# Performance work log

Hardware: AMD Instinct MI355X
Metric: run time of the kernel (lower is better)

The kernel has to match this reference:

```python
import jax, jax.numpy as jnp
import numpy as np

E, T, IN, OUT, GS = 8, 2048, 2048, 2048, 64


def setup_inputs() -> dict:
    key = jax.random.key(0)
    k1, k2, k3, k4, k5 = jax.random.split(key, 5)
    x = jax.random.normal(k1, (T, IN), dtype=jnp.float32)
    # int4 codes in [0,16): stored unpacked as int32 for the reference
    qweight = jax.random.randint(k2, (E, IN, OUT), 0, 16, dtype=jnp.int32)
    G = IN // GS  # quant groups along the reduction dim
    scales = jax.random.uniform(k3, (E, G, OUT), jnp.float32, minval=0.005, maxval=0.02)
    zeros = jax.random.normal(k4, (E, G, OUT), jnp.float32) * 0.01
    scales_and_zeros = jnp.stack([scales, zeros], axis=-1)  # [E, G, OUT, 2]
    # tokens sorted by expert: per-expert counts are diffs of sorted cut points, sum == T
    cuts = jnp.sort(jax.random.randint(k5, (E - 1,), 0, T + 1, dtype=jnp.int32))
    bounds = jnp.concatenate([jnp.zeros((1,), jnp.int32), cuts, jnp.full((1,), T, jnp.int32)])
    tokens_per_expert = jnp.diff(bounds).astype(jnp.int32)  # [E]
    return {
        "x": x,
        "qweight": qweight,
        "scales_and_zeros": scales_and_zeros,
        "tokens_per_expert": tokens_per_expert,
        "group_size": GS,
    }


def reference(x, qweight, scales_and_zeros, tokens_per_expert, group_size):
    """Grouped (per-expert) int4 dequant + GEMM over an expert-sorted token matrix.

    Math of aten._weight_int4pack_mm per expert e over each quant group g:
        W_e[k, n] = (q_e[k, n] - 8) * scale_e[g, n] + zero_e[g, n],  g = k // group_size
        out[rows_e] = x[rows_e] @ W_e
    where rows_e is the contiguous slice given by cumsum(tokens_per_expert).
    """
    n_exp, in_f, out_f = qweight.shape
    n_tok = x.shape[0]
    G = in_f // group_size

    # dequantize all expert weights: [E, IN, OUT]
    q = qweight.reshape(n_exp, G, group_size, out_f).astype(x.dtype)
    scales = scales_and_zeros[..., 0][:, :, None, :]  # [E, G, 1, OUT]
    zeros = scales_and_zeros[..., 1][:, :, None, :]   # [E, G, 1, OUT]
    W = ((q - 8.0) * scales + zeros).reshape(n_exp, in_f, out_f)

    # expert id per token from the cumsum boundaries (tokens are expert-sorted)
    cum = jnp.cumsum(tokens_per_expert)                                # [E]
    eid = jnp.searchsorted(cum, jnp.arange(n_tok), side="right")       # [T]
    onehot = (eid[:, None] == jnp.arange(n_exp)[None, :]).astype(x.dtype)  # [T, E]

    # dispatch -> per-expert GEMM -> combine (jit-safe grouped GEMM)
    xe = jnp.einsum("te,ti->eti", onehot, x)       # [E, T, IN]
    ye = jnp.einsum("eti,eio->eto", xe, W)         # [E, T, OUT]
    out = jnp.einsum("te,eto->to", onehot, ye)     # [T, OUT]
    return out
```

## Files before the change

### kernel.cpp

```cpp
#include <hip/hip_runtime.h>
#include <hip/hip_bf16.h>

constexpr int NE  = 8;
constexpr int T   = 2048;
constexpr int IN  = 2048;
constexpr int OUT = 2048;
constexpr int GS  = 64;
constexpr int G   = IN / GS;

constexpr int BM = 128;
constexpr int BN = 64;
constexpr int BK = 64;
constexpr int KSPLIT = 2;
constexpr int KCH = IN / KSPLIT;
constexpr int LDA = BK + 8;
constexpr int LDB = BK + 8;

using short8  = __attribute__((ext_vector_type(8))) short;
using floatx4 = __attribute__((ext_vector_type(4))) float;

__global__ __launch_bounds__(256, 4)
void hqq_grouped_gemm(const float* __restrict__ x,
                      const int*   __restrict__ qw,
                      const float* __restrict__ snz,
                      const int*   __restrict__ tpe,
                      float* __restrict__ out) {
    const int tid = threadIdx.x;
    const int e   = blockIdx.z >> 1;
    const int kh  = blockIdx.z & 1;
    const int tm  = blockIdx.y;
    const int n0  = blockIdx.x * BN;

    int b0 = 0;
    for (int i = 0; i < NE; ++i) {
        int c = tpe[i];
        if (i < e) b0 += c;
    }
    const int b1 = b0 + tpe[e];
    const int row0 = b0 + tm * BM;
    if (row0 >= b1) return;

    __shared__ __hip_bfloat16 As[BM][LDA];
    __shared__ __hip_bfloat16 Bs[BN][LDB];

    floatx4 acc[2][4];
#pragma unroll
    for (int i = 0; i < 2; ++i)
#pragma unroll
        for (int j = 0; j < 4; ++j)
            acc[i][j] = (floatx4){0.f, 0.f, 0.f, 0.f};

    const int a_c  = (tid & 15) * 4;
    const int a_r0 = tid >> 4;

    const int bn_ = tid & 63;
    const int bk0 = (tid >> 6) * 8;

    const int lane = tid & 63;
    const int wid  = tid >> 6;
    const int wm = wid * 32;
    const int lm = lane & 15;
    const int lk = (lane >> 4) * 8;

    const int*    qbase  = qw + (size_t)e * IN * OUT + n0 + bn_;
    const float2* szbase = (const float2*)snz + (size_t)e * G * OUT + n0 + bn_;

    const int kbeg = kh * KCH;
    const int kend = kbeg + KCH;

    for (int k0 = kbeg; k0 < kend; k0 += BK) {
#pragma unroll
        for (int it = 0; it < 8; ++it) {
            const int r   = a_r0 + it * 16;
            const int row = row0 + r;
            float4 v = {0.f, 0.f, 0.f, 0.f};
            if (row < b1)
                v = *(const float4*)(x + (size_t)row * IN + k0 + a_c);
            union { unsigned long long u; __hip_bfloat162 h2[2]; } pa;
            pa.h2[0] = __float22bfloat162_rn(float2{v.x, v.y});
            pa.h2[1] = __float22bfloat162_rn(float2{v.z, v.w});
            *(unsigned long long*)&As[r][a_c] = pa.u;
        }

        const int g = k0 >> 6;
        const float2 sz = szbase[(size_t)g * OUT];
        const float s = sz.x;
        const float c = sz.y - 8.0f * s;
#pragma unroll
        for (int p = 0; p < 2; ++p) {
            const int k8 = bk0 + p * 32;
            const int* qp = qbase + (size_t)(k0 + k8) * OUT;
            float f[8];
#pragma unroll
            for (int j = 0; j < 8; ++j) {
                const int q = qp[(size_t)j * OUT];
                f[j] = (float)q * s + c;
            }
            union { short8 v; __hip_bfloat162 h2[4]; } pb;
#pragma unroll
            for (int j = 0; j < 4; ++j)
                pb.h2[j] = __float22bfloat162_rn(float2{f[2 * j], f[2 * j + 1]});
            *(short8*)&Bs[bn_][k8] = pb.v;
        }

        __syncthreads();

#pragma unroll
        for (int ks = 0; ks < BK; ks += 32) {
            short8 af[2], bfr[4];
#pragma unroll
            for (int i = 0; i < 2; ++i)
                af[i] = *(const short8*)&As[wm + i * 16 + lm][ks + lk];
#pragma unroll
            for (int j = 0; j < 4; ++j)
                bfr[j] = *(const short8*)&Bs[j * 16 + lm][ks + lk];
#pragma unroll
            for (int i = 0; i < 2; ++i)
#pragma unroll
                for (int j = 0; j < 4; ++j)
                    acc[i][j] = __builtin_amdgcn_mfma_f32_16x16x32_bf16(
                        af[i], bfr[j], acc[i][j], 0, 0, 0);
        }

        __syncthreads();
    }

    const int lq = (lane >> 4) * 4;
#pragma unroll
    for (int i = 0; i < 2; ++i) {
#pragma unroll
        for (int r = 0; r < 4; ++r) {
            const int row = row0 + wm + i * 16 + lq + r;
            if (row < b1) {
                float* op = out + (size_t)row * OUT + n0 + lm;
#pragma unroll
                for (int j = 0; j < 4; ++j)
                    atomicAdd(op + j * 16, acc[i][j][r]);
            }
        }
    }
}

extern "C" void kernel_launch(void* const* d_in, const int* in_sizes, int n_in,
                              void* d_out, int out_size, void* d_ws, size_t ws_size,
                              hipStream_t stream) {
    const float* x   = (const float*)d_in[0];
    const int*   qw  = (const int*)d_in[1];
    const float* snz = (const float*)d_in[2];
    const int*   tpe = (const int*)d_in[3];
    float* out = (float*)d_out;

    hipMemsetAsync(out, 0, (size_t)out_size * sizeof(float), stream);

    dim3 grid(OUT / BN, T / BM, NE * KSPLIT);
    hqq_grouped_gemm<<<grid, 256, 0, stream>>>(x, qw, snz, tpe, out);
}
```

Baseline: 301.5 us.

## Pre-convert activations to bf16, read A fragments directly, prefetch next weight tile

A separate kernel converts x to bf16 in workspace once, so the GEMM no longer reconverts fp32 activations for every N-tile. The GEMM drops the A shared-memory tile and loads A fragments straight from global memory. Int4 weight codes for the next K-tile are loaded into registers before the MFMA work on the current tile, overlapping weight-load latency with compute. The cost is an extra kernel launch, a workspace round-trip, more registers for the prefetch, and uncoalesced, uncached-in-LDS A reads that each wave repeats from global/L2.

```diff
diff --git a/kernel.cpp b/kernel.cpp
--- a/kernel.cpp
+++ b/kernel.cpp
@@ -13,14 +13,23 @@
 constexpr int BK = 64;
 constexpr int KSPLIT = 2;
 constexpr int KCH = IN / KSPLIT;
-constexpr int LDA = BK + 8;
 constexpr int LDB = BK + 8;
 
 using short8  = __attribute__((ext_vector_type(8))) short;
 using floatx4 = __attribute__((ext_vector_type(4))) float;
 
+__global__ __launch_bounds__(256)
+void cvt_x_bf16(const float* __restrict__ x, __hip_bfloat16* __restrict__ xb) {
+    const int i = (blockIdx.x * 256 + threadIdx.x) * 4;
+    const float4 v = *(const float4*)(x + i);
+    union { unsigned long long u; __hip_bfloat162 h2[2]; } p;
+    p.h2[0] = __float22bfloat162_rn(float2{v.x, v.y});
+    p.h2[1] = __float22bfloat162_rn(float2{v.z, v.w});
+    *(unsigned long long*)(xb + i) = p.u;
+}
+
 __global__ __launch_bounds__(256, 4)
-void hqq_grouped_gemm(const float* __restrict__ x,
+void hqq_grouped_gemm(const __hip_bfloat16* __restrict__ xb,
                       const int*   __restrict__ qw,
                       const float* __restrict__ snz,
                       const int*   __restrict__ tpe,
@@ -40,7 +49,6 @@
     const int row0 = b0 + tm * BM;
     if (row0 >= b1) return;
 
-    __shared__ __hip_bfloat16 As[BM][LDA];
     __shared__ __hip_bfloat16 Bs[BN][LDB];
 
     floatx4 acc[2][4];
@@ -49,9 +57,6 @@
 #pragma unroll
         for (int j = 0; j < 4; ++j)
             acc[i][j] = (floatx4){0.f, 0.f, 0.f, 0.f};
-
-    const int a_c  = (tid & 15) * 4;
-    const int a_r0 = tid >> 4;
 
     const int bn_ = tid & 63;
     const int bk0 = (tid >> 6) * 8;
@@ -65,52 +70,56 @@
     const int*    qbase  = qw + (size_t)e * IN * OUT + n0 + bn_;
     const float2* szbase = (const float2*)snz + (size_t)e * G * OUT + n0 + bn_;
 
-    const int kbeg = kh * KCH;
-    const int kend = kbeg + KCH;
+    const int kbeg  = kh * KCH;
+    const int ntile = KCH / BK;
 
-    for (int k0 = kbeg; k0 < kend; k0 += BK) {
-#pragma unroll
-        for (int it = 0; it < 8; ++it) {
-            const int r   = a_r0 + it * 16;
-            const int row = row0 + r;
-            float4 v = {0.f, 0.f, 0.f, 0.f};
-            if (row < b1)
-                v = *(const float4*)(x + (size_t)row * IN + k0 + a_c);
-            union { unsigned long long u; __hip_bfloat162 h2[2]; } pa;
-            pa.h2[0] = __float22bfloat162_rn(float2{v.x, v.y});
-            pa.h2[1] = __float22bfloat162_rn(float2{v.z, v.w});
-            *(unsigned long long*)&As[r][a_c] = pa.u;
-        }
+    int    qv[16];
+    float2 szv;
 
-        const int g = k0 >> 6;
-        const float2 sz = szbase[(size_t)g * OUT];
-        const float s = sz.x;
-        const float c = sz.y - 8.0f * s;
+    auto issue = [&](int k0) {
+        szv = szbase[(size_t)(k0 >> 6) * OUT];
 #pragma unroll
         for (int p = 0; p < 2; ++p) {
-            const int k8 = bk0 + p * 32;
-            const int* qp = qbase + (size_t)(k0 + k8) * OUT;
-            float f[8];
+            const int* qp = qbase + (size_t)(k0 + bk0 + p * 32) * OUT;
 #pragma unroll
-            for (int j = 0; j < 8; ++j) {
-                const int q = qp[(size_t)j * OUT];
-                f[j] = (float)q * s + c;
-            }
+            for (int j = 0; j < 8; ++j)
+                qv[p * 8 + j] = qp[(size_t)j * OUT];
+        }
+    };
+
+    issue(kbeg);
+
+    for (int t = 0; t < ntile; ++t) {
+        const int k0 = kbeg + t * BK;
+
+        const float s = szv.x;
+        const float c = szv.y - 8.0f * s;
+#pragma unroll
+        for (int p = 0; p < 2; ++p) {
             union { short8 v; __hip_bfloat162 h2[4]; } pb;
 #pragma unroll
-            for (int j = 0; j < 4; ++j)
-                pb.h2[j] = __float22bfloat162_rn(float2{f[2 * j], f[2 * j + 1]});
-            *(short8*)&Bs[bn_][k8] = pb.v;
+            for (int j = 0; j < 4; ++j) {
+                const float f0 = (float)qv[p * 8 + 2 * j]     * s + c;
+                const float f1 = (float)qv[p * 8 + 2 * j + 1] * s + c;
+                pb.h2[j] = __float22bfloat162_rn(float2{f0, f1});
+            }
+            *(short8*)&Bs[bn_][bk0 + p * 32] = pb.v;
         }
 
         __syncthreads();
+
+        const int kn = (t + 1 < ntile) ? k0 + BK : k0;
+        issue(kn);
 
 #pragma unroll
         for (int ks = 0; ks < BK; ks += 32) {
             short8 af[2], bfr[4];
 #pragma unroll
-            for (int i = 0; i < 2; ++i)
-                af[i] = *(const short8*)&As[wm + i * 16 + lm][ks + lk];
+            for (int i = 0; i < 2; ++i) {
+                const int row = row0 + wm + i * 16 + lm;
+                const int rr  = row < b1 ? row : (b1 - 1);
+                af[i] = *(const short8*)(xb + (size_t)rr * IN + k0 + ks + lk);
+            }
 #pragma unroll
             for (int j = 0; j < 4; ++j)
                 bfr[j] = *(const short8*)&Bs[j * 16 + lm][ks + lk];
@@ -149,9 +158,12 @@
     const float* snz = (const float*)d_in[2];
     const int*   tpe = (const int*)d_in[3];
     float* out = (float*)d_out;
+    __hip_bfloat16* xb = (__hip_bfloat16*)d_ws;
 
     hipMemsetAsync(out, 0, (size_t)out_size * sizeof(float), stream);
 
+    cvt_x_bf16<<<(T * IN) / (256 * 4), 256, 0, stream>>>(x, xb);
+
     dim3 grid(OUT / BN, T / BM, NE * KSPLIT);
-    hqq_grouped_gemm<<<grid, 256, 0, stream>>>(x, qw, snz, tpe, out);
+    hqq_grouped_gemm<<<grid, 256, 0, stream>>>(xb, qw, snz, tpe, out);
 }
```

New measurement: 268.0 us. 1.12x faster.
